# Kernel tuning notes

Measured on AMD Instinct MI355X. Metric: run time of the kernel, lower is better.

## Reference

```python
import jax, jax.numpy as jnp
import numpy as np

B, T, D, H, A = 1, 262144, 8, 64, 4  # batch, seq_len, state_dim, hidden, n_actions


def setup_inputs() -> dict:
    key = jax.random.key(0)
    ks = jax.random.split(key, 10)
    s = lambda k, shape, sc: jax.random.normal(k, shape, dtype=jnp.float32) * sc
    return {
        "x": jax.random.normal(ks[0], (B, T, D), dtype=jnp.float32),
        # encoder MLP (Dense->tanh, Dense->tanh)
        "W1": s(ks[1], (D, H), 0.5), "b1": jnp.zeros((H,), jnp.float32),
        "W2": s(ks[2], (H, H), 0.15), "b2": jnp.zeros((H,), jnp.float32),
        # SimpleRNN params: h_t = tanh(x_t @ Wx + h_{t-1} @ Wh + b_rnn)
        "Wx": s(ks[3], (H, H), 0.15), "Wh": s(ks[4], (H, H), 0.1),
        "b_rnn": jnp.zeros((H,), jnp.float32),
        # means head
        "Wm": s(ks[5], (H, A), 0.01), "bm": jnp.zeros((A,), jnp.float32),
    }


def reference(x, W1, b1, W2, b2, Wx, Wh, b_rnn, Wm, bm):
    # Masking(mask_value=0): a timestep is masked if ALL features == 0
    mask = jnp.any(x != 0.0, axis=-1)  # [B, T] bool
    # TimeDistributed encoder (applies pointwise over time -> plain batched matmul)
    h1 = jnp.tanh(x @ W1 + b1)          # [B, T, H]
    h2 = jnp.tanh(h1 @ W2 + b2)         # [B, T, H]
    # Precompute input contribution to the RNN outside the scan (efficient form)
    xz = h2 @ Wx + b_rnn                # [B, T, H]

    def step(h, inp):
        z, m = inp                       # z: [B, H], m: [B]
        h_new = jnp.tanh(z + h @ Wh)
        # masked timesteps: carry previous state through (Keras RNN masking semantics)
        h = jnp.where(m[:, None], h_new, h)
        return h, h

    h0 = jnp.zeros((B, H), x.dtype)
    _, hs = jax.lax.scan(step, h0, (jnp.swapaxes(xz, 0, 1), jnp.swapaxes(mask, 0, 1)))
    hs = jnp.swapaxes(hs, 0, 1)          # [B, T, H]
    means = hs @ Wm + bm                 # [B, T, A]
    return means
```

## Files before the change

kernel.cpp:

```cpp
#include <hip/hip_runtime.h>
#include <hip/hip_bf16.h>

constexpr int T_LEN  = 262144;
constexpr int H      = 64;
constexpr int S_LEN  = 8;
constexpr int WARM   = 16;
constexpr int CHUNKS = T_LEN / S_LEN;
constexpr int NWAVE  = CHUNKS / 16;
constexpr int PRE_STRIDE = 68;
constexpr int ZPAD_TAIL = 4;

typedef __attribute__((ext_vector_type(8))) short short8;
typedef __attribute__((ext_vector_type(4))) float f32x4;

__device__ __forceinline__ float fast_tanh(float x) {
    float e = __expf(2.0f * x);
    return 1.0f - 2.0f * __builtin_amdgcn_rcpf(e + 1.0f);
}
__device__ __forceinline__ unsigned short f2bf(float v) {
    unsigned u = __builtin_bit_cast(unsigned, v);
    return (unsigned short)((u + 0x7fffu + ((u >> 16) & 1u)) >> 16);
}
__device__ __forceinline__ float bf2f(unsigned short b) {
    return __builtin_bit_cast(float, (unsigned)b << 16);
}
__device__ __forceinline__ unsigned pack2(float a, float b) {
#if __has_builtin(__builtin_amdgcn_cvt_pk_bf16_f32)
    typedef __attribute__((ext_vector_type(2))) __bf16 bf16x2;
    bf16x2 r = __builtin_amdgcn_cvt_pk_bf16_f32(a, b);
    return __builtin_bit_cast(unsigned, r);
#else
    return (unsigned)f2bf(a) | ((unsigned)f2bf(b) << 16);
#endif
}

__global__ __launch_bounds__(256) void encoder_kernel(
    const float* __restrict__ x,
    const float* __restrict__ W1, const float* __restrict__ b1,
    const float* __restrict__ W2, const float* __restrict__ b2,
    const float* __restrict__ Wx, const float* __restrict__ b_rnn,
    unsigned short* __restrict__ z_s, float* __restrict__ m_s)
{
    __shared__ uint4 w1f[4 * 64];
    __shared__ uint4 w2f[8 * 64];
    __shared__ uint4 w3f[8 * 64];
    __shared__ float pre_[4][16 * PRE_STRIDE];

    const int tid = threadIdx.x;
    const int w   = tid >> 6;
    const int l   = tid & 63;
    const int q   = l >> 4;
    const int l15 = l & 15;

    {
        const int n  = l;
        const int kg = w;
        float v2[16], v3[16];
        #pragma unroll
        for (int kk = 0; kk < 16; ++kk) {
            v2[kk] = W2[(kg * 16 + kk) * 64 + n];
            v3[kk] = Wx[(kg * 16 + kk) * 64 + n];
        }
        const int kh = kg >> 1;
        const int tn = n >> 4;
        #pragma unroll
        for (int s = 0; s < 2; ++s) {
            const int qq   = (2 * kg + s) & 3;
            const int lane = qq * 16 + (n & 15);
            uint4 o2, o3;
            o2.x = pack2(v2[s*8+0], v2[s*8+1]); o2.y = pack2(v2[s*8+2], v2[s*8+3]);
            o2.z = pack2(v2[s*8+4], v2[s*8+5]); o2.w = pack2(v2[s*8+6], v2[s*8+7]);
            o3.x = pack2(v3[s*8+0], v3[s*8+1]); o3.y = pack2(v3[s*8+2], v3[s*8+3]);
            o3.z = pack2(v3[s*8+4], v3[s*8+5]); o3.w = pack2(v3[s*8+6], v3[s*8+7]);
            w2f[(tn * 2 + kh) * 64 + lane] = o2;
            w3f[(tn * 2 + kh) * 64 + lane] = o3;
        }
        uint4 o1 = make_uint4(0, 0, 0, 0);
        if (q < 2) {
            float v1[8];
            #pragma unroll
            for (int j = 0; j < 8; ++j) v1[j] = W1[j * 64 + w * 16 + l15];
            o1.x = pack2(v1[0], v1[1]); o1.y = pack2(v1[2], v1[3]);
            o1.z = pack2(v1[4], v1[5]); o1.w = pack2(v1[6], v1[7]);
        }
        w1f[w * 64 + l] = o1;
    }
    __syncthreads();

    float b1v[4], b2v[4], brv[4];
    #pragma unroll
    for (int tn = 0; tn < 4; ++tn) {
        b1v[tn] = b1[tn * 16 + l15];
        b2v[tn] = b2[tn * 16 + l15];
        brv[tn] = b_rnn[tn * 16 + l15];
    }

    float* mypre = pre_[w];

    float4 xa = make_float4(0.f, 0.f, 0.f, 0.f), xb = xa;
    if (q < 2) {
        const size_t t0 = (size_t)(blockIdx.x * 256 + w * 16 + l15) * 8;
        xa = *(const float4*)(x + t0);
        xb = *(const float4*)(x + t0 + 4);
    }

    #pragma unroll
    for (int it = 0; it < 4; ++it) {
        const int t0w = blockIdx.x * 256 + it * 64 + w * 16;

        float4 na = xa, nb = xb;
        if (it < 3 && q < 2) {
            const size_t tn0 = (size_t)(t0w + 64 + l15) * 8;
            na = *(const float4*)(x + tn0);
            nb = *(const float4*)(x + tn0 + 4);
        }

        short8 a1 = (short8)0;
        if (q < 2) {
            const float xv[8] = {xa.x, xa.y, xa.z, xa.w, xb.x, xb.y, xb.z, xb.w};
            if (q == 0) {
                bool nz = false;
                #pragma unroll
                for (int d = 0; d < 8; ++d) nz = nz || (xv[d] != 0.0f);
                m_s[t0w + l15] = nz ? 1.0f : 0.0f;
                uint4 o;
                o.x = pack2(xv[0], xv[1]); o.y = pack2(xv[2], xv[3]);
                o.z = pack2(xv[4], xv[5]); o.w = pack2(xv[6], xv[7]);
                a1 = __builtin_bit_cast(short8, o);
            } else {
                float lo[8];
                #pragma unroll
                for (int d = 0; d < 8; ++d) lo[d] = xv[d] - bf2f(f2bf(xv[d]));
                uint4 o;
                o.x = pack2(lo[0], lo[1]); o.y = pack2(lo[2], lo[3]);
                o.z = pack2(lo[4], lo[5]); o.w = pack2(lo[6], lo[7]);
                a1 = __builtin_bit_cast(short8, o);
            }
        }

        {
            f32x4 acc[4];
            #pragma unroll
            for (int tn = 0; tn < 4; ++tn)
                acc[tn] = __builtin_amdgcn_mfma_f32_16x16x32_bf16(
                    a1, __builtin_bit_cast(short8, w1f[tn * 64 + l]),
                    (f32x4){0.f, 0.f, 0.f, 0.f}, 0, 0, 0);
            #pragma unroll
            for (int tn = 0; tn < 4; ++tn)
                #pragma unroll
                for (int r = 0; r < 4; ++r)
                    mypre[(q * 4 + r) * PRE_STRIDE + tn * 16 + l15] =
                        fast_tanh(acc[tn][r] + b1v[tn]);
        }
        __builtin_amdgcn_wave_barrier();

        short8 af[2];
        #pragma unroll
        for (int kh = 0; kh < 2; ++kh) {
            const uint4 r0 = *(const uint4*)(mypre + l15 * PRE_STRIDE + kh * 32 + q * 8);
            const uint4 r1 = *(const uint4*)(mypre + l15 * PRE_STRIDE + kh * 32 + q * 8 + 4);
            uint4 p;
            p.x = pack2(__builtin_bit_cast(float, r0.x), __builtin_bit_cast(float, r0.y));
            p.y = pack2(__builtin_bit_cast(float, r0.z), __builtin_bit_cast(float, r0.w));
            p.z = pack2(__builtin_bit_cast(float, r1.x), __builtin_bit_cast(float, r1.y));
            p.w = pack2(__builtin_bit_cast(float, r1.z), __builtin_bit_cast(float, r1.w));
            af[kh] = __builtin_bit_cast(short8, p);
        }
        __builtin_amdgcn_wave_barrier();

        {
            f32x4 acc[4];
            #pragma unroll
            for (int tn = 0; tn < 4; ++tn) {
                f32x4 d = {0.f, 0.f, 0.f, 0.f};
                d = __builtin_amdgcn_mfma_f32_16x16x32_bf16(
                        af[0], __builtin_bit_cast(short8, w2f[(tn * 2 + 0) * 64 + l]), d, 0, 0, 0);
                d = __builtin_amdgcn_mfma_f32_16x16x32_bf16(
                        af[1], __builtin_bit_cast(short8, w2f[(tn * 2 + 1) * 64 + l]), d, 0, 0, 0);
                acc[tn] = d;
            }
            #pragma unroll
            for (int tn = 0; tn < 4; ++tn)
                #pragma unroll
                for (int r = 0; r < 4; ++r)
                    mypre[(q * 4 + r) * PRE_STRIDE + tn * 16 + l15] =
                        fast_tanh(acc[tn][r] + b2v[tn]);
        }
        __builtin_amdgcn_wave_barrier();

        #pragma unroll
        for (int kh = 0; kh < 2; ++kh) {
            const uint4 r0 = *(const uint4*)(mypre + l15 * PRE_STRIDE + kh * 32 + q * 8);
            const uint4 r1 = *(const uint4*)(mypre + l15 * PRE_STRIDE + kh * 32 + q * 8 + 4);
            uint4 p;
            p.x = pack2(__builtin_bit_cast(float, r0.x), __builtin_bit_cast(float, r0.y));
            p.y = pack2(__builtin_bit_cast(float, r0.z), __builtin_bit_cast(float, r0.w));
            p.z = pack2(__builtin_bit_cast(float, r1.x), __builtin_bit_cast(float, r1.y));
            p.w = pack2(__builtin_bit_cast(float, r1.z), __builtin_bit_cast(float, r1.w));
            af[kh] = __builtin_bit_cast(short8, p);
        }
        __builtin_amdgcn_wave_barrier();

        {
            f32x4 acc[4];
            #pragma unroll
            for (int tn = 0; tn < 4; ++tn) {
                f32x4 d = {0.f, 0.f, 0.f, 0.f};
                d = __builtin_amdgcn_mfma_f32_16x16x32_bf16(
                        af[0], __builtin_bit_cast(short8, w3f[(tn * 2 + 0) * 64 + l]), d, 0, 0, 0);
                d = __builtin_amdgcn_mfma_f32_16x16x32_bf16(
                        af[1], __builtin_bit_cast(short8, w3f[(tn * 2 + 1) * 64 + l]), d, 0, 0, 0);
                acc[tn] = d;
            }
            #pragma unroll
            for (int tn = 0; tn < 4; ++tn)
                #pragma unroll
                for (int r = 0; r < 4; ++r)
                    mypre[(q * 4 + r) * PRE_STRIDE + tn * 16 + l15] = acc[tn][r] + brv[tn];
        }
        __builtin_amdgcn_wave_barrier();

        {
            const int ot = l >> 2;
            const int fq = l & 3;
            const float* src = mypre + ot * PRE_STRIDE + fq * 16;
            const uint4 r0 = *(const uint4*)(src + 0);
            const uint4 r1 = *(const uint4*)(src + 4);
            const uint4 r2 = *(const uint4*)(src + 8);
            const uint4 r3 = *(const uint4*)(src + 12);
            uint4 o0, o1;
            o0.x = pack2(__builtin_bit_cast(float, r0.x), __builtin_bit_cast(float, r0.y));
            o0.y = pack2(__builtin_bit_cast(float, r0.z), __builtin_bit_cast(float, r0.w));
            o0.z = pack2(__builtin_bit_cast(float, r1.x), __builtin_bit_cast(float, r1.y));
            o0.w = pack2(__builtin_bit_cast(float, r1.z), __builtin_bit_cast(float, r1.w));
            o1.x = pack2(__builtin_bit_cast(float, r2.x), __builtin_bit_cast(float, r2.y));
            o1.y = pack2(__builtin_bit_cast(float, r2.z), __builtin_bit_cast(float, r2.w));
            o1.z = pack2(__builtin_bit_cast(float, r3.x), __builtin_bit_cast(float, r3.y));
            o1.w = pack2(__builtin_bit_cast(float, r3.z), __builtin_bit_cast(float, r3.w));
            uint4* dst = (uint4*)(z_s + (size_t)(t0w + ot) * 64 + fq * 16);
            dst[0] = o0;
            dst[1] = o1;
        }
        __builtin_amdgcn_wave_barrier();

        xa = na; xb = nb;
    }
}

__global__ __launch_bounds__(256) void rnn_kernel(
    const unsigned short* __restrict__ z_pad, const float* __restrict__ m_pad,
    const float* __restrict__ Wh, const float* __restrict__ Wm,
    const float* __restrict__ bm, float* __restrict__ out)
{
    __shared__ float pre_[4][16 * PRE_STRIDE];

    const int tid = threadIdx.x;
    const int w   = tid >> 6;
    const int l   = tid & 63;
    const int q   = l >> 4;
    const int l15 = l & 15;
    const int rw  = blockIdx.x * 4 + w;
    const int c   = rw * 16 + l15;

    short8 bfrag[8];
    #pragma unroll
    for (int tn = 0; tn < 4; ++tn) {
        #pragma unroll
        for (int kh = 0; kh < 2; ++kh) {
            short8 s;
            #pragma unroll
            for (int j = 0; j < 8; ++j)
                s[j] = (short)f2bf(Wh[(kh * 32 + q * 8 + j) * 64 + tn * 16 + l15]);
            bfrag[tn * 2 + kh] = s;
        }
    }
    short8 wmf[2];
    #pragma unroll
    for (int kh = 0; kh < 2; ++kh) {
        short8 s;
        #pragma unroll
        for (int j = 0; j < 8; ++j)
            s[j] = (l15 < 4) ? (short)f2bf(Wm[(kh * 32 + q * 8 + j) * 4 + l15]) : (short)0;
        wmf[kh] = s;
    }
    const float bm_l = (l15 < 4) ? bm[l15] : 0.0f;

    short8 hfrag[2];
    hfrag[0] = (short8)0;
    hfrag[1] = (short8)0;
    float* mypre = pre_[w];

    const unsigned short* zrow = z_pad + (size_t)c * S_LEN * 64;
    const float*          mrow = m_pad + (size_t)c * S_LEN;
    const int tneg = -(c * S_LEN);

    uint4 zb0[2], zb1[2];
    float mb0, mb1;
    zb0[0] = *(const uint4*)(zrow + q * 8);
    zb0[1] = *(const uint4*)(zrow + 32 + q * 8);
    mb0    = mrow[0];
    zb1[0] = *(const uint4*)(zrow + 64 + q * 8);
    zb1[1] = *(const uint4*)(zrow + 64 + 32 + q * 8);
    mb1    = mrow[1];
    zrow += 128; mrow += 2;

    auto body = [&](uint4* zbuf, float& mref,
                    const unsigned short* zrl, const float* mrl,
                    int stv, bool means_prev, bool may_reset) {
        if (may_reset && rw == 0) {
            if (stv == tneg) { hfrag[0] = (short8)0; hfrag[1] = (short8)0; }
        }
        f32x4 acc[4];
        #pragma unroll
        for (int tn = 0; tn < 4; ++tn) {
            f32x4 d = {0.f, 0.f, 0.f, 0.f};
            d = __builtin_amdgcn_mfma_f32_16x16x32_bf16(hfrag[0], bfrag[tn * 2 + 0], d, 0, 0, 0);
            d = __builtin_amdgcn_mfma_f32_16x16x32_bf16(hfrag[1], bfrag[tn * 2 + 1], d, 0, 0, 0);
            acc[tn] = d;
        }
        if (means_prev) {
            f32x4 a2 = {0.f, 0.f, 0.f, 0.f};
            a2 = __builtin_amdgcn_mfma_f32_16x16x32_bf16(hfrag[0], wmf[0], a2, 0, 0, 0);
            a2 = __builtin_amdgcn_mfma_f32_16x16x32_bf16(hfrag[1], wmf[1], a2, 0, 0, 0);
            if (l15 < 4) {
                #pragma unroll
                for (int r = 0; r < 4; ++r) {
                    const int cm = rw * 16 + q * 4 + r;
                    const size_t tp = (size_t)cm * S_LEN + (stv - 1);
                    out[tp * 4 + l15] = a2[r] + bm_l;
                }
            }
        }
        #pragma unroll
        for (int tn = 0; tn < 4; ++tn)
            #pragma unroll
            for (int r = 0; r < 4; ++r)
                mypre[(q * 4 + r) * PRE_STRIDE + tn * 16 + l15] = acc[tn][r];
        __builtin_amdgcn_wave_barrier();

        #pragma unroll
        for (int kh = 0; kh < 2; ++kh) {
            const unsigned short* zp = (const unsigned short*)&zbuf[kh];
            const uint4 r0 = *(const uint4*)(mypre + l15 * PRE_STRIDE + kh * 32 + q * 8);
            const uint4 r1 = *(const uint4*)(mypre + l15 * PRE_STRIDE + kh * 32 + q * 8 + 4);
            const unsigned pd[8] = {r0.x, r0.y, r0.z, r0.w, r1.x, r1.y, r1.z, r1.w};
            float th[8];
            #pragma unroll
            for (int j = 0; j < 8; ++j)
                th[j] = fast_tanh(__builtin_bit_cast(float, pd[j]) + bf2f(zp[j]));
            uint4 p;
            p.x = pack2(th[0], th[1]); p.y = pack2(th[2], th[3]);
            p.z = pack2(th[4], th[5]); p.w = pack2(th[6], th[7]);
            const short8 ns = __builtin_bit_cast(short8, p);
            hfrag[kh] = (mref != 0.0f) ? ns : hfrag[kh];
        }
        __builtin_amdgcn_wave_barrier();

        zbuf[0] = *(const uint4*)(zrl + q * 8);
        zbuf[1] = *(const uint4*)(zrl + 32 + q * 8);
        mref    = mrl[0];
    };

    for (int i = 0; i < WARM / 2; ++i) {
        const int st = -WARM + 2 * i;
        body(zb0, mb0, zrow,      mrow,     st,     false, true);
        body(zb1, mb1, zrow + 64, mrow + 1, st + 1, false, true);
        zrow += 128; mrow += 2;
    }

    #pragma unroll
    for (int st = 0; st < S_LEN; ++st) {
        if ((st & 1) == 0)
            body(zb0, mb0, zrow + st * 64, mrow + st, st, st >= 1, st == 0);
        else
            body(zb1, mb1, zrow + st * 64, mrow + st, st, true, false);
    }

    {
        f32x4 a2 = {0.f, 0.f, 0.f, 0.f};
        a2 = __builtin_amdgcn_mfma_f32_16x16x32_bf16(hfrag[0], wmf[0], a2, 0, 0, 0);
        a2 = __builtin_amdgcn_mfma_f32_16x16x32_bf16(hfrag[1], wmf[1], a2, 0, 0, 0);
        if (l15 < 4) {
            #pragma unroll
            for (int r = 0; r < 4; ++r) {
                const int cm = rw * 16 + q * 4 + r;
                const size_t tp = (size_t)cm * S_LEN + (S_LEN - 1);
                out[tp * 4 + l15] = a2[r] + bm_l;
            }
        }
    }
}

extern "C" void kernel_launch(void* const* d_in, const int* in_sizes, int n_in,
                              void* d_out, int out_size, void* d_ws, size_t ws_size,
                              hipStream_t stream) {
    const float* x     = (const float*)d_in[0];
    const float* W1    = (const float*)d_in[1];
    const float* b1    = (const float*)d_in[2];
    const float* W2    = (const float*)d_in[3];
    const float* b2    = (const float*)d_in[4];
    const float* Wx    = (const float*)d_in[5];
    const float* Wh    = (const float*)d_in[6];
    const float* b_rnn = (const float*)d_in[7];
    const float* Wm    = (const float*)d_in[8];
    const float* bm    = (const float*)d_in[9];
    float* out = (float*)d_out;

    unsigned short* z_pad = (unsigned short*)d_ws;
    const size_t z_rows   = (size_t)(WARM + T_LEN + ZPAD_TAIL);
    float*          m_pad = (float*)((char*)d_ws + z_rows * H * 2);

    unsigned short* z_s = z_pad + (size_t)WARM * H;
    float*          m_s = m_pad + WARM;

    encoder_kernel<<<T_LEN / 256, 256, 0, stream>>>(x, W1, b1, W2, b2, Wx, b_rnn, z_s, m_s);
    rnn_kernel<<<NWAVE / 4, 256, 0, stream>>>(z_pad, m_pad, Wh, Wm, bm, out);
}
```

Measured before the change: 130.2 us.

## Transpose RNN recurrence MFMA to keep state in registers via bpermute

```diff
diff --git a/kernel.cpp b/kernel.cpp
--- a/kernel.cpp
+++ b/kernel.cpp
@@ -252,17 +252,15 @@
     const float* __restrict__ Wh, const float* __restrict__ Wm,
     const float* __restrict__ bm, float* __restrict__ out)
 {
-    __shared__ float pre_[4][16 * PRE_STRIDE];
-
     const int tid = threadIdx.x;
     const int w   = tid >> 6;
     const int l   = tid & 63;
     const int q   = l >> 4;
-    const int l15 = l & 15;
+    const int n15 = l & 15;
     const int rw  = blockIdx.x * 4 + w;
-    const int c   = rw * 16 + l15;
-
-    short8 bfrag[8];
+    const int c   = rw * 16 + n15;
+
+    short8 afrag[8];
     #pragma unroll
     for (int tn = 0; tn < 4; ++tn) {
         #pragma unroll
@@ -270,8 +268,8 @@
             short8 s;
             #pragma unroll
             for (int j = 0; j < 8; ++j)
-                s[j] = (short)f2bf(Wh[(kh * 32 + q * 8 + j) * 64 + tn * 16 + l15]);
-            bfrag[tn * 2 + kh] = s;
+                s[j] = (short)f2bf(Wh[(kh * 32 + q * 8 + j) * 64 + tn * 16 + n15]);
+            afrag[tn * 2 + kh] = s;
         }
     }
     short8 wmf[2];
@@ -280,85 +278,100 @@
         short8 s;
         #pragma unroll
         for (int j = 0; j < 8; ++j)
-            s[j] = (l15 < 4) ? (short)f2bf(Wm[(kh * 32 + q * 8 + j) * 4 + l15]) : (short)0;
+            s[j] = (n15 < 4) ? (short)f2bf(Wm[(kh * 32 + q * 8 + j) * 4 + n15]) : (short)0;
         wmf[kh] = s;
     }
-    const float bm_l = (l15 < 4) ? bm[l15] : 0.0f;
-
-    short8 hfrag[2];
-    hfrag[0] = (short8)0;
-    hfrag[1] = (short8)0;
-    float* mypre = pre_[w];
+    const float4 bmv = *(const float4*)bm;
+
+    f32x4 hst[4];
+    #pragma unroll
+    for (int tn = 0; tn < 4; ++tn) hst[tn] = (f32x4){0.f, 0.f, 0.f, 0.f};
+    short8 hB[2];
+    hB[0] = (short8)0;
+    hB[1] = (short8)0;
+
+    const int idxA = ((2 * (q & 1) + 0) * 16 + n15) * 4;
+    const int idxB = ((2 * (q & 1) + 1) * 16 + n15) * 4;
+    const bool hiSel = (q >= 2);
 
     const unsigned short* zrow = z_pad + (size_t)c * S_LEN * 64;
     const float*          mrow = m_pad + (size_t)c * S_LEN;
     const int tneg = -(c * S_LEN);
 
-    uint4 zb0[2], zb1[2];
+    uint2 zb0[4], zb1[4];
     float mb0, mb1;
-    zb0[0] = *(const uint4*)(zrow + q * 8);
-    zb0[1] = *(const uint4*)(zrow + 32 + q * 8);
-    mb0    = mrow[0];
-    zb1[0] = *(const uint4*)(zrow + 64 + q * 8);
-    zb1[1] = *(const uint4*)(zrow + 64 + 32 + q * 8);
-    mb1    = mrow[1];
+    #pragma unroll
+    for (int tn = 0; tn < 4; ++tn) {
+        zb0[tn] = *(const uint2*)(zrow + tn * 16 + q * 4);
+        zb1[tn] = *(const uint2*)(zrow + 64 + tn * 16 + q * 4);
+    }
+    mb0 = mrow[0];
+    mb1 = mrow[1];
     zrow += 128; mrow += 2;
 
-    auto body = [&](uint4* zbuf, float& mref,
+    auto body = [&](uint2* zbuf, float& mref,
                     const unsigned short* zrl, const float* mrl,
                     int stv, bool means_prev, bool may_reset) {
         if (may_reset && rw == 0) {
-            if (stv == tneg) { hfrag[0] = (short8)0; hfrag[1] = (short8)0; }
+            if (stv == tneg) {
+                hB[0] = (short8)0; hB[1] = (short8)0;
+                #pragma unroll
+                for (int tn = 0; tn < 4; ++tn) hst[tn] = (f32x4){0.f, 0.f, 0.f, 0.f};
+            }
         }
         f32x4 acc[4];
         #pragma unroll
-        for (int tn = 0; tn < 4; ++tn) {
+        for (int mt = 0; mt < 4; ++mt) {
             f32x4 d = {0.f, 0.f, 0.f, 0.f};
-            d = __builtin_amdgcn_mfma_f32_16x16x32_bf16(hfrag[0], bfrag[tn * 2 + 0], d, 0, 0, 0);
-            d = __builtin_amdgcn_mfma_f32_16x16x32_bf16(hfrag[1], bfrag[tn * 2 + 1], d, 0, 0, 0);
-            acc[tn] = d;
+            d = __builtin_amdgcn_mfma_f32_16x16x32_bf16(afrag[mt * 2 + 0], hB[0], d, 0, 0, 0);
+            d = __builtin_amdgcn_mfma_f32_16x16x32_bf16(afrag[mt * 2 + 1], hB[1], d, 0, 0, 0);
+            acc[mt] = d;
         }
         if (means_prev) {
             f32x4 a2 = {0.f, 0.f, 0.f, 0.f};
-            a2 = __builtin_amdgcn_mfma_f32_16x16x32_bf16(hfrag[0], wmf[0], a2, 0, 0, 0);
-            a2 = __builtin_amdgcn_mfma_f32_16x16x32_bf16(hfrag[1], wmf[1], a2, 0, 0, 0);
-            if (l15 < 4) {
-                #pragma unroll
-                for (int r = 0; r < 4; ++r) {
-                    const int cm = rw * 16 + q * 4 + r;
-                    const size_t tp = (size_t)cm * S_LEN + (stv - 1);
-                    out[tp * 4 + l15] = a2[r] + bm_l;
-                }
-            }
+            a2 = __builtin_amdgcn_mfma_f32_16x16x32_bf16(wmf[0], hB[0], a2, 0, 0, 0);
+            a2 = __builtin_amdgcn_mfma_f32_16x16x32_bf16(wmf[1], hB[1], a2, 0, 0, 0);
+            if (q == 0) {
+                const size_t tp = (size_t)c * S_LEN + (stv - 1);
+                *(float4*)(out + tp * 4) =
+                    make_float4(a2[0] + bmv.x, a2[1] + bmv.y, a2[2] + bmv.z, a2[3] + bmv.w);
+            }
+        }
+        const bool upd = (mref != 0.0f);
+        #pragma unroll
+        for (int tn = 0; tn < 4; ++tn) {
+            const unsigned short* zp = (const unsigned short*)&zbuf[tn];
+            #pragma unroll
+            for (int r = 0; r < 4; ++r) {
+                const float nv = fast_tanh(acc[tn][r] + bf2f(zp[r]));
+                hst[tn][r] = upd ? nv : hst[tn][r];
+            }
+        }
+        unsigned P[4][2];
+        #pragma unroll
+        for (int tn = 0; tn < 4; ++tn) {
+            P[tn][0] = pack2(hst[tn][0], hst[tn][1]);
+            P[tn][1] = pack2(hst[tn][2], hst[tn][3]);
+        }
+        #pragma unroll
+        for (int kh = 0; kh < 2; ++kh) {
+            unsigned fd[4];
+            #pragma unroll
+            for (int d = 0; d < 4; ++d) {
+                const int idx = (d < 2) ? idxA : idxB;
+                const unsigned lo =
+                    (unsigned)__builtin_amdgcn_ds_bpermute(idx, (int)P[2 * kh + 0][d & 1]);
+                const unsigned hi =
+                    (unsigned)__builtin_amdgcn_ds_bpermute(idx, (int)P[2 * kh + 1][d & 1]);
+                fd[d] = hiSel ? hi : lo;
+            }
+            uint4 u = make_uint4(fd[0], fd[1], fd[2], fd[3]);
+            hB[kh] = __builtin_bit_cast(short8, u);
         }
         #pragma unroll
         for (int tn = 0; tn < 4; ++tn)
-            #pragma unroll
-            for (int r = 0; r < 4; ++r)
-                mypre[(q * 4 + r) * PRE_STRIDE + tn * 16 + l15] = acc[tn][r];
-        __builtin_amdgcn_wave_barrier();
-
-        #pragma unroll
-        for (int kh = 0; kh < 2; ++kh) {
-            const unsigned short* zp = (const unsigned short*)&zbuf[kh];
-            const uint4 r0 = *(const uint4*)(mypre + l15 * PRE_STRIDE + kh * 32 + q * 8);
-            const uint4 r1 = *(const uint4*)(mypre + l15 * PRE_STRIDE + kh * 32 + q * 8 + 4);
-            const unsigned pd[8] = {r0.x, r0.y, r0.z, r0.w, r1.x, r1.y, r1.z, r1.w};
-            float th[8];
-            #pragma unroll
-            for (int j = 0; j < 8; ++j)
-                th[j] = fast_tanh(__builtin_bit_cast(float, pd[j]) + bf2f(zp[j]));
-            uint4 p;
-            p.x = pack2(th[0], th[1]); p.y = pack2(th[2], th[3]);
-            p.z = pack2(th[4], th[5]); p.w = pack2(th[6], th[7]);
-            const short8 ns = __builtin_bit_cast(short8, p);
-            hfrag[kh] = (mref != 0.0f) ? ns : hfrag[kh];
-        }
-        __builtin_amdgcn_wave_barrier();
-
-        zbuf[0] = *(const uint4*)(zrl + q * 8);
-        zbuf[1] = *(const uint4*)(zrl + 32 + q * 8);
-        mref    = mrl[0];
+            zbuf[tn] = *(const uint2*)(zrl + tn * 16 + q * 4);
+        mref = mrl[0];
     };
 
     for (int i = 0; i < WARM / 2; ++i) {
@@ -378,15 +391,12 @@
 
     {
         f32x4 a2 = {0.f, 0.f, 0.f, 0.f};
-        a2 = __builtin_amdgcn_mfma_f32_16x16x32_bf16(hfrag[0], wmf[0], a2, 0, 0, 0);
-        a2 = __builtin_amdgcn_mfma_f32_16x16x32_bf16(hfrag[1], wmf[1], a2, 0, 0, 0);
-        if (l15 < 4) {
-            #pragma unroll
-            for (int r = 0; r < 4; ++r) {
-                const int cm = rw * 16 + q * 4 + r;
-                const size_t tp = (size_t)cm * S_LEN + (S_LEN - 1);
-                out[tp * 4 + l15] = a2[r] + bm_l;
-            }
+        a2 = __builtin_amdgcn_mfma_f32_16x16x32_bf16(wmf[0], hB[0], a2, 0, 0, 0);
+        a2 = __builtin_amdgcn_mfma_f32_16x16x32_bf16(wmf[1], hB[1], a2, 0, 0, 0);
+        if (q == 0) {
+            const size_t tp = (size_t)c * S_LEN + (S_LEN - 1);
+            *(float4*)(out + tp * 4) =
+                make_float4(a2[0] + bmv.x, a2[1] + bmv.y, a2[2] + bmv.z, a2[3] + bmv.w);
         }
     }
 }
```

New measurement: 129.5 us. No clear change (-0.5%).
